# Optimization experiments

Measured on AMD Instinct MI355X. Metric: run time of the kernel, lower is better.

Reference implementation:

```python
import jax, jax.numpy as jnp
import numpy as np
from jax import lax

D_MODEL, D_STATE, D_CONV, N_BLOCKS = 128, 32, 8, 6
D_INNER, DT_RANK, K_PRE = 256, 8, 7  # expand=2, dt_rank=ceil(128/16)
BATCH, SEQ = 16, 4096


def setup_inputs() -> dict:
    key = jax.random.key(0)
    ks = jax.random.split(key, 16)
    def rn(k, shape, scale=0.05):
        return jax.random.normal(k, shape, jnp.float32) * scale
    return {
        "x": jax.random.normal(ks[0], (BATCH, SEQ, 1), jnp.float32),
        "pre_conv_w": rn(ks[1], (D_MODEL, 1, K_PRE), 0.3),
        "pre_conv_b": rn(ks[2], (D_MODEL,), 0.01),
        "in_proj_w": rn(ks[3], (N_BLOCKS, 2, 2 * D_INNER, D_MODEL)),
        "conv_w": rn(ks[4], (N_BLOCKS, 2, D_INNER, 1, D_CONV), 0.2),
        "conv_b": rn(ks[5], (N_BLOCKS, 2, D_INNER), 0.01),
        "x_proj_w": rn(ks[6], (N_BLOCKS, 2, DT_RANK + 2 * D_STATE, D_INNER)),
        "dt_proj_w": rn(ks[7], (N_BLOCKS, 2, D_INNER, DT_RANK), 0.1),
        "dt_proj_b": rn(ks[8], (N_BLOCKS, 2, D_INNER), 0.5),
        "A_log": jax.random.uniform(ks[9], (N_BLOCKS, 2, D_INNER, D_STATE), jnp.float32),
        "D_param": rn(ks[10], (N_BLOCKS, 2, D_INNER), 1.0),
        "out_proj_w": rn(ks[11], (N_BLOCKS, 2, D_MODEL, D_INNER)),
        "ln_g": jnp.ones((N_BLOCKS, D_MODEL), jnp.float32),
        "ln_b": jnp.zeros((N_BLOCKS, D_MODEL), jnp.float32),
        "proj_w": rn(ks[12], (1, D_MODEL), 0.1),
        "proj_b": jnp.zeros((1,), jnp.float32),
    }


def _layernorm(x, g, b, eps=1e-5):
    mu = jnp.mean(x, axis=-1, keepdims=True)
    var = jnp.mean(jnp.square(x - mu), axis=-1, keepdims=True)
    return (x - mu) * lax.rsqrt(var + eps) * g + b


def _mamba(x, in_w, cw, cb, xp_w, dt_w, dt_b, a_log, d_par, out_w):
    # x: [B, L, D_MODEL]
    B, L, _ = x.shape
    xz = jnp.einsum('bld,ed->ble', x, in_w)            # [B,L,2*D_INNER]
    u, z = xz[..., :D_INNER], xz[..., D_INNER:]
    # depthwise causal conv over time
    u = lax.conv_general_dilated(
        u.transpose(0, 2, 1), cw, (1,), [(D_CONV - 1, 0)],
        feature_group_count=D_INNER,
        dimension_numbers=('NCH', 'OIH', 'NCH')) + cb[None, :, None]
    u = jax.nn.silu(u).transpose(0, 2, 1)              # [B,L,D_INNER]
    dbc = jnp.einsum('bld,ed->ble', u, xp_w)           # [B,L,DT_RANK+2N]
    dt = jax.nn.softplus(jnp.einsum('blr,dr->bld', dbc[..., :DT_RANK], dt_w) + dt_b)
    Bm = dbc[..., DT_RANK:DT_RANK + D_STATE]           # [B,L,N]
    Cm = dbc[..., DT_RANK + D_STATE:]                  # [B,L,N]
    A = -jnp.exp(a_log)                                # [D_INNER,N]

    def step(h, inp):
        dt_t, B_t, C_t, u_t = inp                      # [B,d],[B,n],[B,n],[B,d]
        dA = jnp.exp(dt_t[..., None] * A)              # [B,d,n]
        h = h * dA + (dt_t * u_t)[..., None] * B_t[:, None, :]
        y = jnp.einsum('bdn,bn->bd', h, C_t)
        return h, y

    h0 = jnp.zeros((B, D_INNER, D_STATE), x.dtype)
    _, ys = lax.scan(step, h0, (dt.transpose(1, 0, 2), Bm.transpose(1, 0, 2),
                                Cm.transpose(1, 0, 2), u.transpose(1, 0, 2)))
    y = ys.transpose(1, 0, 2) + u * d_par              # [B,L,D_INNER]
    y = y * jax.nn.silu(z)
    return jnp.einsum('ble,de->bld', y, out_w)         # [B,L,D_MODEL]


def reference(x, pre_conv_w, pre_conv_b, in_proj_w, conv_w, conv_b, x_proj_w,
              dt_proj_w, dt_proj_b, A_log, D_param, out_proj_w, ln_g, ln_b,
              proj_w, proj_b):
    pad = K_PRE // 2
    h = lax.conv_general_dilated(
        x.transpose(0, 2, 1), pre_conv_w, (1,), [(pad, pad)],
        dimension_numbers=('NCH', 'OIH', 'NCH')) + pre_conv_b[None, :, None]
    h = jax.nn.gelu(h, approximate=False).transpose(0, 2, 1)  # [B,L,D_MODEL]
    for i in range(N_BLOCKS):
        f = _mamba(h, in_proj_w[i, 0], conv_w[i, 0], conv_b[i, 0], x_proj_w[i, 0],
                   dt_proj_w[i, 0], dt_proj_b[i, 0], A_log[i, 0], D_param[i, 0],
                   out_proj_w[i, 0])
        hb = jnp.flip(h, axis=1)
        b = _mamba(hb, in_proj_w[i, 1], conv_w[i, 1], conv_b[i, 1], x_proj_w[i, 1],
                   dt_proj_w[i, 1], dt_proj_b[i, 1], A_log[i, 1], D_param[i, 1],
                   out_proj_w[i, 1])
        b = jnp.flip(b, axis=1)
        out = (f + b) * 0.5
        h = _layernorm(out + h, ln_g[i], ln_b[i])  # dropout: eval mode (identity)
    y = jnp.einsum('bld,od->blo', h, proj_w) + proj_b
    return y[..., 0]  # [B, L]
```

## Files before the change

kernel.cpp:

```cpp
#include <hip/hip_runtime.h>
#include <hip/hip_bf16.h>
#include <cstdint>
#include <cstddef>

#define L_SEQ   4096
#define BATCH_N 16
#define BLTOK   (BATCH_N * L_SEQ)
#define DMODEL  128
#define DINNER  256
#define DSTATE  32
#define DTRANK  8

#define LC  64
#define GCH 64
#define LOG2E 1.44269504088896340736f

typedef _Float16 half8 __attribute__((ext_vector_type(8)));
typedef float    floatx4 __attribute__((ext_vector_type(4)));

#define LDSW 40

__global__ __launch_bounds__(128) void pre_conv_gelu(
    const float* __restrict__ x,
    const float* __restrict__ w,
    const float* __restrict__ bias,
    float* __restrict__ h,
    _Float16* __restrict__ hb)
{
    int r = blockIdx.x;
    int c = threadIdx.x;
    int b = r >> 12;
    int l = r & 4095;
    float acc = bias[c];
    const float* wp = w + c * 7;
#pragma unroll
    for (int k = 0; k < 7; ++k) {
        int ll = l + k - 3;
        if (ll >= 0 && ll < L_SEQ)
            acc += x[(size_t)(b << 12) + ll] * wp[k];
    }
    float ge = 0.5f * acc * (1.f + erff(acc * 0.70710678118654752f));
    h[(size_t)r * DMODEL + c]  = ge;
    hb[(size_t)r * DMODEL + c] = (_Float16)ge;
}

__global__ __launch_bounds__(256) void cvt_weights(
    const float* __restrict__ inw,  _Float16* __restrict__ inwh,
    const float* __restrict__ xpw,  _Float16* __restrict__ xpwh,
    const float* __restrict__ outw, _Float16* __restrict__ outwh)
{
    int i = blockIdx.x * 256 + threadIdx.x;
    if (i < 12 * 512 * 128) inwh[i]  = (_Float16)inw[i];
    if (i < 12 * 72 * 256)  xpwh[i]  = (_Float16)xpw[i];
    if (i < 12 * 128 * 256) outwh[i] = (_Float16)outw[i];
}

__global__ __launch_bounds__(256) void gemm_mfma(
    const _Float16* __restrict__ A, int lda,
    const _Float16* __restrict__ W, int ldw,
    float* __restrict__ Out,
    _Float16* __restrict__ U16,
    __hip_bfloat16* __restrict__ Zb,
    int N, int K, int rev, int mode)
{
    __shared__ __align__(16) _Float16 As[64 * LDSW];
    __shared__ __align__(16) _Float16 Ws[64 * LDSW];

    int tid  = threadIdx.x;
    int wave = tid >> 6;
    int lane = tid & 63;
    int m0 = blockIdx.y * 64;
    int n0 = blockIdx.x * 64;

    int srow = tid >> 2;
    int skc  = (tid & 3) * 8;

    int garow = m0 + srow;
    if (rev) { int bb = garow >> 12; int ll = garow & 4095; garow = (bb << 12) + (4095 - ll); }
    const _Float16* Aptr = A + (size_t)garow * lda + skc;
    int wrow = n0 + srow;
    bool wok = (wrow < N);
    const _Float16* Wptr = W + (size_t)(wok ? wrow : 0) * ldw + skc;

    int lr = lane & 15;
    int lk = (lane >> 4) * 8;
    int soff = srow * LDSW + skc;
    int aoff = (16 * wave + lr) * LDSW + lk;

    floatx4 acc0 = {0.f, 0.f, 0.f, 0.f};
    floatx4 acc1 = acc0, acc2 = acc0, acc3 = acc0;

    for (int k0 = 0; k0 < K; k0 += 32) {
        half8 av = *(const half8*)(Aptr + k0);
        half8 bv = {};
        if (wok) bv = *(const half8*)(Wptr + k0);
        __syncthreads();
        *(half8*)&As[soff] = av;
        *(half8*)&Ws[soff] = bv;
        __syncthreads();
        half8 af = *(const half8*)&As[aoff];
        half8 b0 = *(const half8*)&Ws[( 0 + lr) * LDSW + lk];
        half8 b1 = *(const half8*)&Ws[(16 + lr) * LDSW + lk];
        half8 b2 = *(const half8*)&Ws[(32 + lr) * LDSW + lk];
        half8 b3 = *(const half8*)&Ws[(48 + lr) * LDSW + lk];
        acc0 = __builtin_amdgcn_mfma_f32_16x16x32_f16(af, b0, acc0, 0, 0, 0);
        acc1 = __builtin_amdgcn_mfma_f32_16x16x32_f16(af, b1, acc1, 0, 0, 0);
        acc2 = __builtin_amdgcn_mfma_f32_16x16x32_f16(af, b2, acc2, 0, 0, 0);
        acc3 = __builtin_amdgcn_mfma_f32_16x16x32_f16(af, b3, acc3, 0, 0, 0);
    }

    int orow = m0 + 16 * wave + (lane >> 4) * 4;
    floatx4 av4[4] = {acc0, acc1, acc2, acc3};
#pragma unroll
    for (int jb = 0; jb < 4; ++jb) {
        int col = n0 + jb * 16 + lr;
#pragma unroll
        for (int r = 0; r < 4; ++r) {
            int row = orow + r;
            float v = av4[jb][r];
            if (mode == 0) {
                if (col < N) Out[(size_t)row * 72 + col] = v;
            } else if (mode == 1) {
                if (col < 256) U16[(size_t)row * 256 + col] = (_Float16)v;
                else Zb[(size_t)row * 256 + (col - 256)] = __float2bfloat16(v);
            } else if (mode == 2) {
                Out[(size_t)row * 128 + col] = v;
            } else {
                int bb = row >> 12, ll = row & 4095;
                size_t o = ((size_t)(bb << 12) + (4095 - ll)) * 128 + col;
                Out[o] = 0.5f * (Out[o] + v);
            }
        }
    }
}

__global__ __launch_bounds__(256) void dwconv_silu(
    const _Float16* __restrict__ u,
    const float* __restrict__ cw,
    const float* __restrict__ cb,
    _Float16* __restrict__ uc)
{
    int b  = blockIdx.x >> 7;
    int lt = blockIdx.x & 127;
    int l0 = lt * 32;
    int d  = threadIdx.x;

    float wv[8];
    const float* wp = cw + d * 8;
#pragma unroll
    for (int k = 0; k < 8; ++k) wv[k] = wp[k];
    float bias = cb[d];

    size_t rowb = (size_t)(b << 12);
    float win[8];
#pragma unroll
    for (int j = 0; j < 7; ++j) {
        int ll = l0 - 7 + j;
        win[j] = (ll >= 0) ? (float)u[(rowb + ll) * DINNER + d] : 0.f;
    }
#pragma unroll
    for (int i = 0; i < 32; ++i) {
        int l = l0 + i;
        win[7] = (float)u[(rowb + l) * DINNER + d];
        float acc = bias;
#pragma unroll
        for (int j = 0; j < 8; ++j) acc += win[j] * wv[j];
        float s = acc / (1.f + __expf(-acc));
        uc[(rowb + l) * DINNER + d] = (_Float16)s;
#pragma unroll
        for (int j = 0; j < 7; ++j) win[j] = win[j + 1];
    }
}

__global__ __launch_bounds__(256, 4) void scan_phase1(
    const float* __restrict__ dbc,
    const _Float16* __restrict__ u,
    float* __restrict__ aggh,
    float* __restrict__ aggs,
    const float* __restrict__ dt_w,
    const float* __restrict__ dt_b,
    const float* __restrict__ a_log)
{
    __shared__ __align__(16) float sh[LC * 72];
    int bg = blockIdx.x;
    int b  = bg >> 6;
    int g  = bg & (GCH - 1);
    int d  = threadIdx.x;

    size_t base = (size_t)b * L_SEQ + (size_t)g * LC;
    {
        const float4* src4 = (const float4*)(dbc + base * 72);
        float4* dst4 = (float4*)sh;
        for (int i = d; i < LC * 18; i += 256) dst4[i] = src4[i];
    }

    const float* wr = dt_w + d * DTRANK;
    float w0 = wr[0], w1 = wr[1], w2 = wr[2], w3 = wr[3];
    float w4 = wr[4], w5 = wr[5], w6 = wr[6], w7 = wr[7];
    float bias = dt_b[d];

    float al2[32];
    {
        const float4* ar = (const float4*)(a_log + d * DSTATE);
#pragma unroll
        for (int k = 0; k < 8; ++k) {
            float4 v = ar[k];
            al2[4 * k + 0] = -__expf(v.x) * LOG2E;
            al2[4 * k + 1] = -__expf(v.y) * LOG2E;
            al2[4 * k + 2] = -__expf(v.z) * LOG2E;
            al2[4 * k + 3] = -__expf(v.w) * LOG2E;
        }
    }
    __syncthreads();

    float h[32];
#pragma unroll
    for (int n = 0; n < 32; ++n) h[n] = 0.f;
    float S = 0.f;

    for (int t = 0; t < LC; ++t) {
        const float* row = sh + t * 72;
        float4 r0 = *(const float4*)row;
        float4 r1 = *(const float4*)(row + 4);
        float dtr = bias + r0.x * w0 + r0.y * w1 + r0.z * w2 + r0.w * w3
                         + r1.x * w4 + r1.y * w5 + r1.z * w6 + r1.w * w7;
        float dtv = (dtr > 15.f) ? dtr : __logf(1.f + __expf(dtr));
        S += dtv;
        float du = dtv * (float)u[(base + t) * DINNER + d];
#pragma unroll
        for (int n = 0; n < 32; n += 4) {
            float4 Bv = *(const float4*)(row + 8 + n);
            h[n + 0] = h[n + 0] * __builtin_amdgcn_exp2f(dtv * al2[n + 0]) + du * Bv.x;
            h[n + 1] = h[n + 1] * __builtin_amdgcn_exp2f(dtv * al2[n + 1]) + du * Bv.y;
            h[n + 2] = h[n + 2] * __builtin_amdgcn_exp2f(dtv * al2[n + 2]) + du * Bv.z;
            h[n + 3] = h[n + 3] * __builtin_amdgcn_exp2f(dtv * al2[n + 3]) + du * Bv.w;
        }
    }

    size_t ob = ((size_t)(b * GCH + g) * 32) * 256 + d;
#pragma unroll
    for (int n = 0; n < 32; ++n) aggh[ob + (size_t)n * 256] = h[n];
    aggs[(size_t)(b * GCH + g) * 256 + d] = S;
}

__global__ __launch_bounds__(256) void scan_phase2(
    float* __restrict__ aggh,
    const float* __restrict__ aggs,
    const float* __restrict__ a_log)
{
    int b = blockIdx.x >> 5;
    int n = blockIdx.x & 31;
    int d = threadIdx.x;

    float a = -__expf(a_log[d * DSTATE + n]);
    float hrun = 0.f;
    for (int g = 0; g < GCH; ++g) {
        size_t os = (size_t)(b * GCH + g) * 256 + d;
        size_t oh = ((size_t)(b * GCH + g) * 32 + n) * 256 + d;
        float S  = aggs[os];
        float he = aggh[oh];
        aggh[oh] = hrun;
        hrun = hrun * __expf(a * S) + he;
    }
}

__global__ __launch_bounds__(256, 4) void scan_phase3(
    const float* __restrict__ dbc,
    const _Float16* __restrict__ u,
    const __hip_bfloat16* __restrict__ z_in,
    _Float16* __restrict__ y_out,
    const float* __restrict__ aggh,
    const float* __restrict__ dt_w,
    const float* __restrict__ dt_b,
    const float* __restrict__ a_log,
    const float* __restrict__ Dp)
{
    __shared__ __align__(16) float sh[LC * 72];
    int bg = blockIdx.x;
    int b  = bg >> 6;
    int g  = bg & (GCH - 1);
    int d  = threadIdx.x;

    size_t base = (size_t)b * L_SEQ + (size_t)g * LC;
    {
        const float4* src4 = (const float4*)(dbc + base * 72);
        float4* dst4 = (float4*)sh;
        for (int i = d; i < LC * 18; i += 256) dst4[i] = src4[i];
    }

    const float* wr = dt_w + d * DTRANK;
    float w0 = wr[0], w1 = wr[1], w2 = wr[2], w3 = wr[3];
    float w4 = wr[4], w5 = wr[5], w6 = wr[6], w7 = wr[7];
    float bias = dt_b[d];
    float Dd = Dp[d];

    float al2[32];
    {
        const float4* ar = (const float4*)(a_log + d * DSTATE);
#pragma unroll
        for (int k = 0; k < 8; ++k) {
            float4 v = ar[k];
            al2[4 * k + 0] = -__expf(v.x) * LOG2E;
            al2[4 * k + 1] = -__expf(v.y) * LOG2E;
            al2[4 * k + 2] = -__expf(v.z) * LOG2E;
            al2[4 * k + 3] = -__expf(v.w) * LOG2E;
        }
    }

    float h[32];
    size_t ob = ((size_t)(b * GCH + g) * 32) * 256 + d;
#pragma unroll
    for (int n = 0; n < 32; ++n) h[n] = aggh[ob + (size_t)n * 256];

    __syncthreads();

    for (int t = 0; t < LC; ++t) {
        const float* row = sh + t * 72;
        float4 r0 = *(const float4*)row;
        float4 r1 = *(const float4*)(row + 4);
        float dtr = bias + r0.x * w0 + r0.y * w1 + r0.z * w2 + r0.w * w3
                         + r1.x * w4 + r1.y * w5 + r1.z * w6 + r1.w * w7;
        float dtv = (dtr > 15.f) ? dtr : __logf(1.f + __expf(dtr));
        float uv = (float)u[(base + t) * DINNER + d];
        float du = dtv * uv;
        float zv = __bfloat162float(z_in[(base + t) * DINNER + d]);

        float y = 0.f;
#pragma unroll
        for (int n = 0; n < 32; n += 4) {
            float4 Bv = *(const float4*)(row + 8 + n);
            float4 Cv = *(const float4*)(row + 40 + n);
            h[n + 0] = h[n + 0] * __builtin_amdgcn_exp2f(dtv * al2[n + 0]) + du * Bv.x;
            h[n + 1] = h[n + 1] * __builtin_amdgcn_exp2f(dtv * al2[n + 1]) + du * Bv.y;
            h[n + 2] = h[n + 2] * __builtin_amdgcn_exp2f(dtv * al2[n + 2]) + du * Bv.z;
            h[n + 3] = h[n + 3] * __builtin_amdgcn_exp2f(dtv * al2[n + 3]) + du * Bv.w;
            y += h[n + 0] * Cv.x + h[n + 1] * Cv.y
               + h[n + 2] * Cv.z + h[n + 3] * Cv.w;
        }
        float yv = y + uv * Dd;
        float sig = 1.f / (1.f + __expf(-zv));
        y_out[(base + t) * DINNER + d] = (_Float16)(yv * (zv * sig));
    }
}

__global__ __launch_bounds__(128) void combine_ln(
    const float* __restrict__ osum,
    float* __restrict__ h,
    _Float16* __restrict__ hb,
    const float* __restrict__ g,
    const float* __restrict__ be)
{
    __shared__ float red[128];
    int r = blockIdx.x;
    int c = threadIdx.x;
    size_t idx = (size_t)r * DMODEL + c;

    float v = osum[idx] + h[idx];

    red[c] = v;
    __syncthreads();
    for (int s = 64; s > 0; s >>= 1) {
        if (c < s) red[c] += red[c + s];
        __syncthreads();
    }
    float mu = red[0] * (1.f / 128.f);
    __syncthreads();
    float dv = v - mu;
    red[c] = dv * dv;
    __syncthreads();
    for (int s = 64; s > 0; s >>= 1) {
        if (c < s) red[c] += red[c + s];
        __syncthreads();
    }
    float var = red[0] * (1.f / 128.f);
    float o = dv * rsqrtf(var + 1e-5f) * g[c] + be[c];
    h[idx]  = o;
    hb[idx] = (_Float16)o;
}

__global__ __launch_bounds__(128) void final_proj(
    const float* __restrict__ h,
    const float* __restrict__ pw,
    const float* __restrict__ pb,
    float* __restrict__ out)
{
    __shared__ float red[128];
    int r = blockIdx.x;
    int c = threadIdx.x;
    red[c] = h[(size_t)r * DMODEL + c] * pw[c];
    __syncthreads();
    for (int s = 64; s > 0; s >>= 1) {
        if (c < s) red[c] += red[c + s];
        __syncthreads();
    }
    if (c == 0) out[r] = red[0] + pb[0];
}

extern "C" void kernel_launch(void* const* d_in, const int* in_sizes, int n_in,
                              void* d_out, int out_size, void* d_ws, size_t ws_size,
                              hipStream_t stream)
{
    const float* x    = (const float*)d_in[0];
    const float* pcw  = (const float*)d_in[1];
    const float* pcb  = (const float*)d_in[2];
    const float* inw  = (const float*)d_in[3];
    const float* cw   = (const float*)d_in[4];
    const float* cb   = (const float*)d_in[5];
    const float* xpw  = (const float*)d_in[6];
    const float* dtw  = (const float*)d_in[7];
    const float* dtb  = (const float*)d_in[8];
    const float* alog = (const float*)d_in[9];
    const float* dpar = (const float*)d_in[10];
    const float* outw = (const float*)d_in[11];
    const float* lng  = (const float*)d_in[12];
    const float* lnb  = (const float*)d_in[13];
    const float* pw   = (const float*)d_in[14];
    const float* pb   = (const float*)d_in[15];
    float* out = (float*)d_out;

    float* h  = (float*)d_ws;
    float* A  = h + (size_t)BLTOK * 128;
    __hip_bfloat16* zy = (__hip_bfloat16*)(A + (size_t)BLTOK * 256);
    _Float16* ucb = (_Float16*)((char*)zy + (size_t)BLTOK * 256 * 2);
    _Float16* hb  = (_Float16*)((char*)ucb + (size_t)BLTOK * 256 * 2);
    float* E  = (float*)((char*)hb + (size_t)BLTOK * 128 * 2);
    _Float16* inwh  = (_Float16*)(E + (size_t)BLTOK * 128);
    _Float16* xpwh  = inwh + (size_t)12 * 512 * 128;
    _Float16* outwh = xpwh + (size_t)12 * 72 * 256;
    float* aggs = (float*)(outwh + (size_t)12 * 128 * 256);
    _Float16* u16 = (_Float16*)A;
    float* dbc  = A;
    float* aggh = A + (size_t)BLTOK * 128;

    cvt_weights<<<(12 * 512 * 128 + 255) / 256, 256, 0, stream>>>(
        inw, inwh, xpw, xpwh, outw, outwh);
    pre_conv_gelu<<<BLTOK, 128, 0, stream>>>(x, pcw, pcb, h, hb);

    for (int blk = 0; blk < 6; ++blk) {
        for (int dir = 0; dir < 2; ++dir) {
            int s = blk * 2 + dir;
            gemm_mfma<<<dim3(8, BLTOK / 64), 256, 0, stream>>>(
                hb, DMODEL, inwh + (size_t)s * 512 * 128, 128,
                nullptr, u16, zy, 512, 128, dir, 1);
            dwconv_silu<<<16 * 128, 256, 0, stream>>>(
                u16, cw + (size_t)s * 256 * 8, cb + (size_t)s * 256, ucb);
            gemm_mfma<<<dim3(2, BLTOK / 64), 256, 0, stream>>>(
                ucb, DINNER, xpwh + (size_t)s * 72 * 256, 256,
                dbc, nullptr, nullptr, 72, 256, 0, 0);
            scan_phase1<<<16 * GCH, 256, 0, stream>>>(
                dbc, ucb, aggh, aggs,
                dtw + (size_t)s * 256 * 8, dtb + (size_t)s * 256,
                alog + (size_t)s * 256 * 32);
            scan_phase2<<<16 * 32, 256, 0, stream>>>(
                aggh, aggs, alog + (size_t)s * 256 * 32);
            scan_phase3<<<16 * GCH, 256, 0, stream>>>(
                dbc, ucb, zy, (_Float16*)zy, aggh,
                dtw + (size_t)s * 256 * 8, dtb + (size_t)s * 256,
                alog + (size_t)s * 256 * 32, dpar + (size_t)s * 256);
            gemm_mfma<<<dim3(2, BLTOK / 64), 256, 0, stream>>>(
                (const _Float16*)zy, DINNER, outwh + (size_t)s * 128 * 256, 256,
                E, nullptr, nullptr, 128, 256, 0, 2 + dir);
        }
        combine_ln<<<BLTOK, 128, 0, stream>>>(
            E, h, hb, lng + blk * 128, lnb + blk * 128);
    }

    final_proj<<<BLTOK, 128, 0, stream>>>(h, pw, pb, out);
}
```

Before: 4.427 ms.

## Split scan state dimension across two half-waves to double scan parallelism

Scan phases 1 and 3 now give each channel to two lanes, with each lane handling 16 of the 32 state entries, and launch twice as many blocks, each covering 128 channels. Phase 3 combines the partial C-dot results with a cross-half shuffle, and only one half writes the output. The goal is to halve per-thread registers and serial work so that occupancy rises (launch bounds go from 4 to 6) and more work runs in parallel on the sequential scan. In exchange, the dt/softplus computation and the u and z loads are now done twice per channel, the shared dbc tile is loaded twice as often across blocks, and per-step output stores are half-masked.

```diff
diff --git a/kernel.cpp b/kernel.cpp
--- a/kernel.cpp
+++ b/kernel.cpp
@@ -172,7 +172,7 @@
     }
 }
 
-__global__ __launch_bounds__(256, 4) void scan_phase1(
+__global__ __launch_bounds__(256, 6) void scan_phase1(
     const float* __restrict__ dbc,
     const _Float16* __restrict__ u,
     float* __restrict__ aggh,
@@ -183,15 +183,21 @@
 {
     __shared__ __align__(16) float sh[LC * 72];
     int bg = blockIdx.x;
-    int b  = bg >> 6;
     int g  = bg & (GCH - 1);
-    int d  = threadIdx.x;
+    int dg = (bg >> 6) & 1;
+    int b  = bg >> 7;
+    int tid  = threadIdx.x;
+    int wave = tid >> 6;
+    int lane = tid & 63;
+    int half = lane >> 5;
+    int d    = dg * 128 + wave * 32 + (lane & 31);
+    int n0   = half * 16;
 
     size_t base = (size_t)b * L_SEQ + (size_t)g * LC;
     {
         const float4* src4 = (const float4*)(dbc + base * 72);
         float4* dst4 = (float4*)sh;
-        for (int i = d; i < LC * 18; i += 256) dst4[i] = src4[i];
+        for (int i = tid; i < LC * 18; i += 256) dst4[i] = src4[i];
     }
 
     const float* wr = dt_w + d * DTRANK;
@@ -199,11 +205,11 @@
     float w4 = wr[4], w5 = wr[5], w6 = wr[6], w7 = wr[7];
     float bias = dt_b[d];
 
-    float al2[32];
+    float al2[16];
     {
-        const float4* ar = (const float4*)(a_log + d * DSTATE);
-#pragma unroll
-        for (int k = 0; k < 8; ++k) {
+        const float4* ar = (const float4*)(a_log + d * DSTATE + n0);
+#pragma unroll
+        for (int k = 0; k < 4; ++k) {
             float4 v = ar[k];
             al2[4 * k + 0] = -__expf(v.x) * LOG2E;
             al2[4 * k + 1] = -__expf(v.y) * LOG2E;
@@ -213,9 +219,9 @@
     }
     __syncthreads();
 
-    float h[32];
-#pragma unroll
-    for (int n = 0; n < 32; ++n) h[n] = 0.f;
+    float h[16];
+#pragma unroll
+    for (int n = 0; n < 16; ++n) h[n] = 0.f;
     float S = 0.f;
 
     for (int t = 0; t < LC; ++t) {
@@ -228,8 +234,8 @@
         S += dtv;
         float du = dtv * (float)u[(base + t) * DINNER + d];
 #pragma unroll
-        for (int n = 0; n < 32; n += 4) {
-            float4 Bv = *(const float4*)(row + 8 + n);
+        for (int n = 0; n < 16; n += 4) {
+            float4 Bv = *(const float4*)(row + 8 + n0 + n);
             h[n + 0] = h[n + 0] * __builtin_amdgcn_exp2f(dtv * al2[n + 0]) + du * Bv.x;
             h[n + 1] = h[n + 1] * __builtin_amdgcn_exp2f(dtv * al2[n + 1]) + du * Bv.y;
             h[n + 2] = h[n + 2] * __builtin_amdgcn_exp2f(dtv * al2[n + 2]) + du * Bv.z;
@@ -237,10 +243,11 @@
         }
     }
 
-    size_t ob = ((size_t)(b * GCH + g) * 32) * 256 + d;
-#pragma unroll
-    for (int n = 0; n < 32; ++n) aggh[ob + (size_t)n * 256] = h[n];
-    aggs[(size_t)(b * GCH + g) * 256 + d] = S;
+    size_t ob = ((size_t)(b * GCH + g) * 32 + n0) * 256 + d;
+#pragma unroll
+    for (int n = 0; n < 16; ++n) aggh[ob + (size_t)n * 256] = h[n];
+    if (half == 0)
+        aggs[(size_t)(b * GCH + g) * 256 + d] = S;
 }
 
 __global__ __launch_bounds__(256) void scan_phase2(
@@ -264,7 +271,7 @@
     }
 }
 
-__global__ __launch_bounds__(256, 4) void scan_phase3(
+__global__ __launch_bounds__(256, 6) void scan_phase3(
     const float* __restrict__ dbc,
     const _Float16* __restrict__ u,
     const __hip_bfloat16* __restrict__ z_in,
@@ -277,15 +284,21 @@
 {
     __shared__ __align__(16) float sh[LC * 72];
     int bg = blockIdx.x;
-    int b  = bg >> 6;
     int g  = bg & (GCH - 1);
-    int d  = threadIdx.x;
+    int dg = (bg >> 6) & 1;
+    int b  = bg >> 7;
+    int tid  = threadIdx.x;
+    int wave = tid >> 6;
+    int lane = tid & 63;
+    int half = lane >> 5;
+    int d    = dg * 128 + wave * 32 + (lane & 31);
+    int n0   = half * 16;
 
     size_t base = (size_t)b * L_SEQ + (size_t)g * LC;
     {
         const float4* src4 = (const float4*)(dbc + base * 72);
         float4* dst4 = (float4*)sh;
-        for (int i = d; i < LC * 18; i += 256) dst4[i] = src4[i];
+        for (int i = tid; i < LC * 18; i += 256) dst4[i] = src4[i];
     }
 
     const float* wr = dt_w + d * DTRANK;
@@ -294,11 +307,11 @@
     float bias = dt_b[d];
     float Dd = Dp[d];
 
-    float al2[32];
+    float al2[16];
     {
-        const float4* ar = (const float4*)(a_log + d * DSTATE);
-#pragma unroll
-        for (int k = 0; k < 8; ++k) {
+        const float4* ar = (const float4*)(a_log + d * DSTATE + n0);
+#pragma unroll
+        for (int k = 0; k < 4; ++k) {
             float4 v = ar[k];
             al2[4 * k + 0] = -__expf(v.x) * LOG2E;
             al2[4 * k + 1] = -__expf(v.y) * LOG2E;
@@ -307,10 +320,10 @@
         }
     }
 
-    float h[32];
-    size_t ob = ((size_t)(b * GCH + g) * 32) * 256 + d;
-#pragma unroll
-    for (int n = 0; n < 32; ++n) h[n] = aggh[ob + (size_t)n * 256];
+    float h[16];
+    size_t ob = ((size_t)(b * GCH + g) * 32 + n0) * 256 + d;
+#pragma unroll
+    for (int n = 0; n < 16; ++n) h[n] = aggh[ob + (size_t)n * 256];
 
     __syncthreads();
 
@@ -325,21 +338,25 @@
         float du = dtv * uv;
         float zv = __bfloat162float(z_in[(base + t) * DINNER + d]);
 
-        float y = 0.f;
-#pragma unroll
-        for (int n = 0; n < 32; n += 4) {
-            float4 Bv = *(const float4*)(row + 8 + n);
-            float4 Cv = *(const float4*)(row + 40 + n);
+        float p = 0.f;
+#pragma unroll
+        for (int n = 0; n < 16; n += 4) {
+            float4 Bv = *(const float4*)(row + 8 + n0 + n);
+            float4 Cv = *(const float4*)(row + 40 + n0 + n);
             h[n + 0] = h[n + 0] * __builtin_amdgcn_exp2f(dtv * al2[n + 0]) + du * Bv.x;
             h[n + 1] = h[n + 1] * __builtin_amdgcn_exp2f(dtv * al2[n + 1]) + du * Bv.y;
             h[n + 2] = h[n + 2] * __builtin_amdgcn_exp2f(dtv * al2[n + 2]) + du * Bv.z;
             h[n + 3] = h[n + 3] * __builtin_amdgcn_exp2f(dtv * al2[n + 3]) + du * Bv.w;
-            y += h[n + 0] * Cv.x + h[n + 1] * Cv.y
+            p += h[n + 0] * Cv.x + h[n + 1] * Cv.y
                + h[n + 2] * Cv.z + h[n + 3] * Cv.w;
         }
-        float yv = y + uv * Dd;
-        float sig = 1.f / (1.f + __expf(-zv));
-        y_out[(base + t) * DINNER + d] = (_Float16)(yv * (zv * sig));
+        p += __shfl_xor(p, 32);
+
+        if (half == 0) {
+            float yv = p + uv * Dd;
+            float sig = 1.f / (1.f + __expf(-zv));
+            y_out[(base + t) * DINNER + d] = (_Float16)(yv * (zv * sig));
+        }
     }
 }
 
@@ -447,13 +464,13 @@
             gemm_mfma<<<dim3(2, BLTOK / 64), 256, 0, stream>>>(
                 ucb, DINNER, xpwh + (size_t)s * 72 * 256, 256,
                 dbc, nullptr, nullptr, 72, 256, 0, 0);
-            scan_phase1<<<16 * GCH, 256, 0, stream>>>(
+            scan_phase1<<<16 * 2 * GCH, 256, 0, stream>>>(
                 dbc, ucb, aggh, aggs,
                 dtw + (size_t)s * 256 * 8, dtb + (size_t)s * 256,
                 alog + (size_t)s * 256 * 32);
             scan_phase2<<<16 * 32, 256, 0, stream>>>(
                 aggh, aggs, alog + (size_t)s * 256 * 32);
-            scan_phase3<<<16 * GCH, 256, 0, stream>>>(
+            scan_phase3<<<16 * 2 * GCH, 256, 0, stream>>>(
                 dbc, ucb, zy, (_Float16*)zy, aggh,
                 dtw + (size_t)s * 256 * 8, dtb + (size_t)s * 256,
                 alog + (size_t)s * 256 * 32, dpar + (size_t)s * 256);
```

After: 4.595 ms. 1.04x slower.
